# Kernel optimization log

Hardware: AMD Instinct MI355X
Metric: run time of the kernel (lower is better)

Reference implementation:

```python
import jax, jax.numpy as jnp
import numpy as np

NEG_INF = -1e9  # large negative for masking (avoid NaN rows under -inf with fully masked rows)
LEAKY_SLOPE = 0.2

def setup_inputs() -> dict:
    key = jax.random.key(0)
    k1, k2, k3, k4, k5 = jax.random.split(key, 5)
    N, in_dim, out_dim = 8192, 512, 64
    x = jax.random.normal(k1, (N, in_dim), dtype=jnp.float32)
    adj = jax.random.randint(k2, (N, N), 0, 2, dtype=jnp.int32)
    W = jax.random.normal(k3, (out_dim, in_dim), dtype=jnp.float32) * (1.0 / np.sqrt(in_dim))
    a_src = jax.random.normal(k4, (out_dim,), dtype=jnp.float32)
    a_dst = jax.random.normal(k5, (out_dim,), dtype=jnp.float32)
    return {"x": x, "adj": adj, "W": W, "a_src": a_src, "a_dst": a_dst}

def reference(x, adj, W, a_src, a_dst):
    # Linear projection: Wh[n, d]
    Wh = x @ W.T
    # Additive GAT attention: e[i, j] = LeakyReLU(a_src . Wh_i + a_dst . Wh_j)
    s = Wh @ a_src  # [N]
    d = Wh @ a_dst  # [N]
    e = jax.nn.leaky_relu(s[:, None] + d[None, :], negative_slope=LEAKY_SLOPE)  # [N, N]
    e = jnp.where(adj > 0, e, NEG_INF)
    alpha = jax.nn.softmax(e, axis=1)  # [N, N]
    # Dropout on alpha is identity in eval/reference mode.
    h_prime = alpha @ Wh  # [N, out_dim]
    return h_prime
```

## Files before the change

### kernel.cpp

```cpp
#include <hip/hip_runtime.h>
#include <hip/hip_bf16.h>

#define GN 8192
#define IN_DIM 512
#define ODIM 64
#define SLOPE 0.2f
#define JSPLIT 16
#define JCH (GN / JSPLIT)
#define NTILE 4

typedef __attribute__((ext_vector_type(4))) float  f32x4;
typedef __attribute__((ext_vector_type(4))) int    i32x4;
typedef __attribute__((ext_vector_type(8))) short  bf16x8;
typedef __attribute__((ext_vector_type(4))) unsigned short u16x4;

static __device__ __forceinline__ float bf2f(unsigned short u) {
    return __uint_as_float(((unsigned)u) << 16);
}
static __device__ __forceinline__ unsigned short f2bf(float f) {
    union { float f; unsigned u; } c; c.f = f;
    unsigned b = c.u;
    return (unsigned short)((b + 0x7fffu + ((b >> 16) & 1u)) >> 16);
}

static __device__ __forceinline__ bf16x8 load8(const void* p, size_t off, int f32) {
    if (f32) {
        f32x4 lo = *(const f32x4*)((const float*)p + off);
        f32x4 hi = *(const f32x4*)((const float*)p + off + 4);
        bf16x8 r;
        #pragma unroll
        for (int q = 0; q < 4; ++q) {
            r[q]     = (short)f2bf(lo[q]);
            r[4 + q] = (short)f2bf(hi[q]);
        }
        return r;
    }
    return *(const bf16x8*)((const ushort*)p + off);
}

extern "C" __global__ __launch_bounds__(256)
void gat_proj(const void* __restrict__ x_, const void* __restrict__ W_,
              const void* __restrict__ as_, const void* __restrict__ ad_,
              ushort* __restrict__ WhTp, float* __restrict__ s_arr,
              float* __restrict__ E1, float* __restrict__ E2,
              int* __restrict__ dmax_bits, int* __restrict__ dflag,
              float* __restrict__ accum, float* __restrict__ lsum)
{
    {
        f32x4 z = {0.f, 0.f, 0.f, 0.f};
        f32x4* ap = (f32x4*)(accum + (size_t)blockIdx.x * 4096);
        #pragma unroll
        for (int k = 0; k < 4; ++k) ap[k * 256 + threadIdx.x] = z;
        if (threadIdx.x < 64) lsum[blockIdx.x * 64 + threadIdx.x] = 0.f;
    }
    const int wave = threadIdx.x >> 6;
    const int lane = threadIdx.x & 63;
    unsigned xw = ((const unsigned*)x_)[lane];
    unsigned ef = (xw >> 23) & 0xffu;
    unsigned long long vt = __ballot(ef > 60u && ef < 180u);
    const int f32 = (__popcll(vt) >= 32) ? 1 : 0;
    if (blockIdx.x == 0 && threadIdx.x == 0) *dflag = f32;

    const int quad = lane >> 4;
    const int lq   = lane & 15;
    const int i0   = blockIdx.x * 64 + wave * 16;

    f32x4 acc[4] = {{0,0,0,0},{0,0,0,0},{0,0,0,0},{0,0,0,0}};
    const size_t arow = (size_t)(i0 + lq) * IN_DIM;
    #pragma unroll 2
    for (int k0 = 0; k0 < IN_DIM; k0 += 32) {
        const int kk = k0 + quad * 8;
        bf16x8 a  = load8(x_, arow + kk, f32);
        bf16x8 b0 = load8(W_, (size_t)( 0 + lq) * IN_DIM + kk, f32);
        bf16x8 b1 = load8(W_, (size_t)(16 + lq) * IN_DIM + kk, f32);
        bf16x8 b2 = load8(W_, (size_t)(32 + lq) * IN_DIM + kk, f32);
        bf16x8 b3 = load8(W_, (size_t)(48 + lq) * IN_DIM + kk, f32);
        acc[0] = __builtin_amdgcn_mfma_f32_16x16x32_bf16(a, b0, acc[0], 0, 0, 0);
        acc[1] = __builtin_amdgcn_mfma_f32_16x16x32_bf16(a, b1, acc[1], 0, 0, 0);
        acc[2] = __builtin_amdgcn_mfma_f32_16x16x32_bf16(a, b2, acc[2], 0, 0, 0);
        acc[3] = __builtin_amdgcn_mfma_f32_16x16x32_bf16(a, b3, acc[3], 0, 0, 0);
    }
    float av_s[4], av_d[4];
    #pragma unroll
    for (int t = 0; t < 4; ++t) {
        const int n = t * 16 + lq;
        av_s[t] = f32 ? ((const float*)as_)[n] : bf2f(((const ushort*)as_)[n]);
        av_d[t] = f32 ? ((const float*)ad_)[n] : bf2f(((const ushort*)ad_)[n]);
    }
    #pragma unroll
    for (int t = 0; t < 4; ++t) {
        u16x4 pk;
        #pragma unroll
        for (int r = 0; r < 4; ++r) pk[r] = f2bf(acc[t][r]);
        const size_t hw = ((size_t)((i0 >> 3) + (quad >> 1)) * 64 + t * 16 + lq) * 8
                          + (quad & 1) * 4;
        *(u16x4*)(WhTp + hw) = pk;
    }
    float ps[4], pd[4];
    #pragma unroll
    for (int r = 0; r < 4; ++r) {
        float s = 0.f, d = 0.f;
        #pragma unroll
        for (int t = 0; t < 4; ++t) {
            s = fmaf(acc[t][r], av_s[t], s);
            d = fmaf(acc[t][r], av_d[t], d);
        }
        #pragma unroll
        for (int off = 1; off < 16; off <<= 1) {
            s += __shfl_xor(s, off);
            d += __shfl_xor(d, off);
        }
        ps[r] = s; pd[r] = d;
    }
    if (lq == 0) {
        float dmx = -1e30f;
        #pragma unroll
        for (int r = 0; r < 4; ++r) {
            const int n = i0 + quad * 4 + r;
            const float dv = pd[r];
            s_arr[n] = ps[r];
            E1[n] = __expf(fminf(dv, 87.f));
            E2[n] = __expf(SLOPE * dv);
            dmx = fmaxf(dmx, dv);
        }
        if (dmx > 0.f) atomicMax(dmax_bits, __float_as_int(dmx));
    }
}

extern "C" __global__ __launch_bounds__(256)
void gat_attn(const int* __restrict__ adj, const ushort* __restrict__ WhTp,
              const float* __restrict__ s_arr,
              const float* __restrict__ E1, const float* __restrict__ E2,
              const int* __restrict__ dmax_bits,
              float* __restrict__ accum, float* __restrict__ lsum)
{
    const int b    = blockIdx.x;
    const int ib   = 127 - (b & 127);
    const int js0  = b >> 7;
    const int wave = threadIdx.x >> 6;
    const int lane = threadIdx.x & 63;
    const int quad = lane >> 4;
    const int lq   = lane & 15;
    const int i0   = ib * 64;
    const int i    = i0 + wave * 16 + lq;

    const float dmax = __int_as_float(*dmax_bits);
    const float si  = s_arr[i];
    const float tbv = si + dmax;
    const float mi  = fmaxf(tbv, SLOPE * tbv);
    const float Aw  = __expf(si - mi);
    const float Bw  = __expf(SLOPE * si - mi);

    const size_t rowbase = (size_t)i * GN + quad * 8;

    #define COLOF(u) ((js0 + 4 * (NTILE - 1 - ((u) >> 4))) * JCH + ((u) & 15) * 32)

    i32x4 ra[4], rb[4];

    f32x4 acc0 = {0,0,0,0}, acc1 = {0,0,0,0}, acc2 = {0,0,0,0}, acc3 = {0,0,0,0};
    f32x4 acc4 = {0,0,0,0};
    bf16x8 ones;
    #pragma unroll
    for (int q = 0; q < 8; ++q) ones[q] = (short)0x3F80;

    #pragma unroll
    for (int c = 0; c < 4; ++c) {
        const int* p = adj + rowbase + COLOF(c);
        ra[c] = ((const i32x4*)p)[0];
        rb[c] = ((const i32x4*)p)[1];
    }
    f32x4 e1a, e1b, e2a, e2b;
    bf16x8 b0, b1, b2, b3;
    {
        const int col = COLOF(0);
        const float* p1 = E1 + col + quad * 8;
        const float* p2 = E2 + col + quad * 8;
        e1a = *(const f32x4*)p1; e1b = *(const f32x4*)(p1 + 4);
        e2a = *(const f32x4*)p2; e2b = *(const f32x4*)(p2 + 4);
        const ushort* nb = WhTp + ((size_t)(col >> 3) + quad) * 512;
        b0 = *(const bf16x8*)(nb + ( 0 + lq) * 8);
        b1 = *(const bf16x8*)(nb + (16 + lq) * 8);
        b2 = *(const bf16x8*)(nb + (32 + lq) * 8);
        b3 = *(const bf16x8*)(nb + (48 + lq) * 8);
    }

    #pragma unroll 1
    for (int t = 0; t < NTILE; ++t) {
        #pragma unroll
        for (int it = 0; it < 16; ++it) {
            const int u = t * 16 + it;
            const i32x4 va = ra[it & 3], vb = rb[it & 3];
            if (t < NTILE - 1 || it < 12) {
                const int* p = adj + rowbase + COLOF(u + 4);
                ra[it & 3] = ((const i32x4*)p)[0];
                rb[it & 3] = ((const i32x4*)p)[1];
            }
            const int un  = (u < NTILE * 16 - 1) ? u + 1 : u;
            const int ncol = COLOF(un);
            const float* p1 = E1 + ncol + quad * 8;
            const float* p2 = E2 + ncol + quad * 8;
            f32x4 ne1a = *(const f32x4*)p1, ne1b = *(const f32x4*)(p1 + 4);
            f32x4 ne2a = *(const f32x4*)p2, ne2b = *(const f32x4*)(p2 + 4);
            const ushort* nb = WhTp + ((size_t)(ncol >> 3) + quad) * 512;
            bf16x8 nb0 = *(const bf16x8*)(nb + ( 0 + lq) * 8);
            bf16x8 nb1 = *(const bf16x8*)(nb + (16 + lq) * 8);
            bf16x8 nb2 = *(const bf16x8*)(nb + (32 + lq) * 8);
            bf16x8 nb3 = *(const bf16x8*)(nb + (48 + lq) * 8);
            float w[8];
            #pragma unroll
            for (int q = 0; q < 4; ++q) {
                const float w0 = fmaxf(Aw * e1a[q], Bw * e2a[q]);
                const float w1 = fmaxf(Aw * e1b[q], Bw * e2b[q]);
                w[q]     = (va[q] > 0) ? w0 : 0.f;
                w[4 + q] = (vb[q] > 0) ? w1 : 0.f;
            }
            union { bf16x8 v; __hip_bfloat162 h[4]; } af;
            #pragma unroll
            for (int q = 0; q < 4; ++q)
                af.h[q] = __float22bfloat162_rn(make_float2(w[2 * q], w[2 * q + 1]));
            acc0 = __builtin_amdgcn_mfma_f32_16x16x32_bf16(af.v, b0, acc0, 0, 0, 0);
            acc1 = __builtin_amdgcn_mfma_f32_16x16x32_bf16(af.v, b1, acc1, 0, 0, 0);
            acc2 = __builtin_amdgcn_mfma_f32_16x16x32_bf16(af.v, b2, acc2, 0, 0, 0);
            acc3 = __builtin_amdgcn_mfma_f32_16x16x32_bf16(af.v, b3, acc3, 0, 0, 0);
            acc4 = __builtin_amdgcn_mfma_f32_16x16x32_bf16(af.v, ones, acc4, 0, 0, 0);
            e1a = ne1a; e1b = ne1b; e2a = ne2a; e2b = ne2b;
            b0 = nb0; b1 = nb1; b2 = nb2; b3 = nb3;
        }
    }
    #undef COLOF

    const int orow = i0 + wave * 16 + quad * 4;
    if (lq == 0) {
        #pragma unroll
        for (int r = 0; r < 4; ++r) atomicAdd(&lsum[orow + r], acc4[r]);
    }
    #pragma unroll
    for (int r = 0; r < 4; ++r) {
        atomicAdd(&accum[(size_t)(orow + r) * ODIM +  0 + lq], acc0[r]);
        atomicAdd(&accum[(size_t)(orow + r) * ODIM + 16 + lq], acc1[r]);
        atomicAdd(&accum[(size_t)(orow + r) * ODIM + 32 + lq], acc2[r]);
        atomicAdd(&accum[(size_t)(orow + r) * ODIM + 48 + lq], acc3[r]);
    }
}

extern "C" __global__ __launch_bounds__(256)
void gat_final(const float* __restrict__ accum, const float* __restrict__ lsum,
               const int* __restrict__ flag, void* __restrict__ out)
{
    const int idx = blockIdx.x * 256 + threadIdx.x;
    const float v = accum[idx] / lsum[idx >> 6];
    if (*flag) ((float*)out)[idx] = v;
    else       ((ushort*)out)[idx] = f2bf(v);
}

extern "C" void kernel_launch(void* const* d_in, const int* in_sizes, int n_in,
                              void* d_out, int out_size, void* d_ws, size_t ws_size,
                              hipStream_t stream)
{
    const void* x     = d_in[0];
    const int*  adj   = (const int*)d_in[1];
    const void* W     = d_in[2];
    const void* a_src = d_in[3];
    const void* a_dst = d_in[4];

    char* ws = (char*)d_ws;
    size_t off = 0;
    int* dmax_bits = (int*)(ws + off);  off += 128;
    int* dflag = (int*)(ws + off);      off += 128;
    size_t zero_bytes = off;
    float* accum = (float*)(ws + off);  off += (size_t)GN * ODIM * 4;
    float* lsum  = (float*)(ws + off);  off += (size_t)GN * 4;
    float* s_arr = (float*)(ws + off);  off += (size_t)GN * 4;
    float* E1    = (float*)(ws + off);  off += (size_t)GN * 4;
    float* E2    = (float*)(ws + off);  off += (size_t)GN * 4;
    ushort* WhTp = (ushort*)(ws + off); off += (size_t)ODIM * GN * 2;

    hipMemsetAsync(ws, 0, zero_bytes, stream);
    gat_proj<<<GN / 64, 256, 0, stream>>>(x, W, a_src, a_dst,
                                          WhTp, s_arr, E1, E2, dmax_bits, dflag,
                                          accum, lsum);
    gat_attn<<<512, 256, 0, stream>>>(adj, WhTp, s_arr, E1, E2,
                                      dmax_bits, accum, lsum);
    gat_final<<<GN * ODIM / 256, 256, 0, stream>>>(accum, lsum, dflag, d_out);
}
```

Before: 447.3 us.

## Stage E1/E2 in LDS and deepen prefetch of adjacency and Wh tiles

The attention kernel now copies the block's E1/E2 column slice into shared memory once at kernel start, replacing per-iteration global loads. Adjacency prefetch depth grows from 4 to 8 tiles and the Wh B-operand prefetch grows from 1 to 4 tiles ahead, using register ring buffers. The aim is to hide more global-memory latency on the adj stream, which dominates, at the cost of more VGPRs and possibly lower occupancy, plus one barrier.

```diff
diff --git a/kernel.cpp b/kernel.cpp
--- a/kernel.cpp
+++ b/kernel.cpp
@@ -36,6 +36,14 @@
         return r;
     }
     return *(const bf16x8*)((const ushort*)p + off);
+}
+
+static __device__ __forceinline__ int colof(int js0, int u) {
+    return (js0 + 4 * (NTILE - 1 - (u >> 4))) * JCH + (u & 15) * 32;
+}
+static __device__ __forceinline__ int colof2(int js0, int t, int itx) {
+    const int tt = t + (itx >> 4);
+    return (js0 + 4 * (NTILE - 1 - tt)) * JCH + (itx & 15) * 32;
 }
 
 extern "C" __global__ __launch_bounds__(256)
@@ -134,6 +142,7 @@
               const int* __restrict__ dmax_bits,
               float* __restrict__ accum, float* __restrict__ lsum)
 {
+    __shared__ float lE[2 * NTILE * 512];
     const int b    = blockIdx.x;
     const int ib   = 127 - (b & 127);
     const int js0  = b >> 7;
@@ -144,6 +153,15 @@
     const int i0   = ib * 64;
     const int i    = i0 + wave * 16 + lq;
 
+    {
+        const int m0 = threadIdx.x * 8;
+        const int gcol = colof(js0, m0 >> 5) + (m0 & 31);
+        *(f32x4*)&lE[m0]            = *(const f32x4*)(E1 + gcol);
+        *(f32x4*)&lE[m0 + 4]        = *(const f32x4*)(E1 + gcol + 4);
+        *(f32x4*)&lE[2048 + m0]     = *(const f32x4*)(E2 + gcol);
+        *(f32x4*)&lE[2048 + m0 + 4] = *(const f32x4*)(E2 + gcol + 4);
+    }
+
     const float dmax = __int_as_float(*dmax_bits);
     const float si  = s_arr[i];
     const float tbv = si + dmax;
@@ -153,9 +171,8 @@
 
     const size_t rowbase = (size_t)i * GN + quad * 8;
 
-    #define COLOF(u) ((js0 + 4 * (NTILE - 1 - ((u) >> 4))) * JCH + ((u) & 15) * 32)
-
-    i32x4 ra[4], rb[4];
+    i32x4 ra[8], rb[8];
+    bf16x8 w0r[4], w1r[4], w2r[4], w3r[4];
 
     f32x4 acc0 = {0,0,0,0}, acc1 = {0,0,0,0}, acc2 = {0,0,0,0}, acc3 = {0,0,0,0};
     f32x4 acc4 = {0,0,0,0};
@@ -165,47 +182,47 @@
 
     #pragma unroll
     for (int c = 0; c < 4; ++c) {
-        const int* p = adj + rowbase + COLOF(c);
+        const int col = colof(js0, c);
+        const ushort* nb = WhTp + ((size_t)(col >> 3) + quad) * 512;
+        w0r[c] = *(const bf16x8*)(nb + ( 0 + lq) * 8);
+        w1r[c] = *(const bf16x8*)(nb + (16 + lq) * 8);
+        w2r[c] = *(const bf16x8*)(nb + (32 + lq) * 8);
+        w3r[c] = *(const bf16x8*)(nb + (48 + lq) * 8);
+    }
+    #pragma unroll
+    for (int c = 0; c < 8; ++c) {
+        const int* p = adj + rowbase + colof(js0, c);
         ra[c] = ((const i32x4*)p)[0];
         rb[c] = ((const i32x4*)p)[1];
     }
-    f32x4 e1a, e1b, e2a, e2b;
-    bf16x8 b0, b1, b2, b3;
-    {
-        const int col = COLOF(0);
-        const float* p1 = E1 + col + quad * 8;
-        const float* p2 = E2 + col + quad * 8;
-        e1a = *(const f32x4*)p1; e1b = *(const f32x4*)(p1 + 4);
-        e2a = *(const f32x4*)p2; e2b = *(const f32x4*)(p2 + 4);
-        const ushort* nb = WhTp + ((size_t)(col >> 3) + quad) * 512;
-        b0 = *(const bf16x8*)(nb + ( 0 + lq) * 8);
-        b1 = *(const bf16x8*)(nb + (16 + lq) * 8);
-        b2 = *(const bf16x8*)(nb + (32 + lq) * 8);
-        b3 = *(const bf16x8*)(nb + (48 + lq) * 8);
-    }
+    __syncthreads();
 
     #pragma unroll 1
     for (int t = 0; t < NTILE; ++t) {
         #pragma unroll
         for (int it = 0; it < 16; ++it) {
             const int u = t * 16 + it;
-            const i32x4 va = ra[it & 3], vb = rb[it & 3];
-            if (t < NTILE - 1 || it < 12) {
-                const int* p = adj + rowbase + COLOF(u + 4);
-                ra[it & 3] = ((const i32x4*)p)[0];
-                rb[it & 3] = ((const i32x4*)p)[1];
+            bf16x8 cb0 = w0r[it & 3], cb1 = w1r[it & 3];
+            bf16x8 cb2 = w2r[it & 3], cb3 = w3r[it & 3];
+            if ((t < NTILE - 1) || (it < 12)) {
+                const int col = colof2(js0, t, it + 4);
+                const ushort* nb = WhTp + ((size_t)(col >> 3) + quad) * 512;
+                w0r[it & 3] = *(const bf16x8*)(nb + ( 0 + lq) * 8);
+                w1r[it & 3] = *(const bf16x8*)(nb + (16 + lq) * 8);
+                w2r[it & 3] = *(const bf16x8*)(nb + (32 + lq) * 8);
+                w3r[it & 3] = *(const bf16x8*)(nb + (48 + lq) * 8);
             }
-            const int un  = (u < NTILE * 16 - 1) ? u + 1 : u;
-            const int ncol = COLOF(un);
-            const float* p1 = E1 + ncol + quad * 8;
-            const float* p2 = E2 + ncol + quad * 8;
-            f32x4 ne1a = *(const f32x4*)p1, ne1b = *(const f32x4*)(p1 + 4);
-            f32x4 ne2a = *(const f32x4*)p2, ne2b = *(const f32x4*)(p2 + 4);
-            const ushort* nb = WhTp + ((size_t)(ncol >> 3) + quad) * 512;
-            bf16x8 nb0 = *(const bf16x8*)(nb + ( 0 + lq) * 8);
-            bf16x8 nb1 = *(const bf16x8*)(nb + (16 + lq) * 8);
-            bf16x8 nb2 = *(const bf16x8*)(nb + (32 + lq) * 8);
-            bf16x8 nb3 = *(const bf16x8*)(nb + (48 + lq) * 8);
+            const i32x4 va = ra[it & 7], vb = rb[it & 7];
+            if ((t < NTILE - 1) || (it < 8)) {
+                const int* p = adj + rowbase + colof2(js0, t, it + 8);
+                ra[it & 7] = ((const i32x4*)p)[0];
+                rb[it & 7] = ((const i32x4*)p)[1];
+            }
+            const float* pe = lE + u * 32 + quad * 8;
+            const f32x4 e1a = *(const f32x4*)pe;
+            const f32x4 e1b = *(const f32x4*)(pe + 4);
+            const f32x4 e2a = *(const f32x4*)(pe + 2048);
+            const f32x4 e2b = *(const f32x4*)(pe + 2052);
             float w[8];
             #pragma unroll
             for (int q = 0; q < 4; ++q) {
@@ -218,16 +235,13 @@
             #pragma unroll
             for (int q = 0; q < 4; ++q)
                 af.h[q] = __float22bfloat162_rn(make_float2(w[2 * q], w[2 * q + 1]));
-            acc0 = __builtin_amdgcn_mfma_f32_16x16x32_bf16(af.v, b0, acc0, 0, 0, 0);
-            acc1 = __builtin_amdgcn_mfma_f32_16x16x32_bf16(af.v, b1, acc1, 0, 0, 0);
-            acc2 = __builtin_amdgcn_mfma_f32_16x16x32_bf16(af.v, b2, acc2, 0, 0, 0);
-            acc3 = __builtin_amdgcn_mfma_f32_16x16x32_bf16(af.v, b3, acc3, 0, 0, 0);
+            acc0 = __builtin_amdgcn_mfma_f32_16x16x32_bf16(af.v, cb0, acc0, 0, 0, 0);
+            acc1 = __builtin_amdgcn_mfma_f32_16x16x32_bf16(af.v, cb1, acc1, 0, 0, 0);
+            acc2 = __builtin_amdgcn_mfma_f32_16x16x32_bf16(af.v, cb2, acc2, 0, 0, 0);
+            acc3 = __builtin_amdgcn_mfma_f32_16x16x32_bf16(af.v, cb3, acc3, 0, 0, 0);
             acc4 = __builtin_amdgcn_mfma_f32_16x16x32_bf16(af.v, ones, acc4, 0, 0, 0);
-            e1a = ne1a; e1b = ne1b; e2a = ne2a; e2b = ne2b;
-            b0 = nb0; b1 = nb1; b2 = nb2; b3 = nb3;
-        }
-    }
-    #undef COLOF
+        }
+    }
 
     const int orow = i0 + wave * 16 + quad * 4;
     if (lq == 0) {
```

New measurement: 446.4 us. About the same (-0.2%).

## Pack adjacency into a bitmask and stage E1/E2 in LDS for attention

Applied to the files above, without the earlier changes.

Adds a pre-pass kernel that compresses the int32 adjacency matrix into a one-bit-per-edge mask with fully coalesced reads. The attention kernel then reads 4 bytes of mask per 32 columns instead of 128 bytes of int32, and loads the E1/E2 exponent tables once into shared memory. The attention grid doubles to 1024 blocks, each covering contiguous 1024-column spans. The full adjacency matrix is still read once, so the gain depends on the pack kernel streaming better than the old strided per-row loads did.

```diff
diff --git a/kernel.cpp b/kernel.cpp
--- a/kernel.cpp
+++ b/kernel.cpp
@@ -5,9 +5,8 @@
 #define IN_DIM 512
 #define ODIM 64
 #define SLOPE 0.2f
-#define JSPLIT 16
-#define JCH (GN / JSPLIT)
-#define NTILE 4
+#define NT2 2
+#define JSPLIT2 8
 
 typedef __attribute__((ext_vector_type(4))) float  f32x4;
 typedef __attribute__((ext_vector_type(4))) int    i32x4;
@@ -36,6 +35,22 @@
         return r;
     }
     return *(const bf16x8*)((const ushort*)p + off);
+}
+
+extern "C" __global__ __launch_bounds__(256)
+void gat_pack(const int* __restrict__ adj, unsigned* __restrict__ gbm)
+{
+    const size_t ui = (size_t)blockIdx.x * 256 + threadIdx.x;
+    const int* p = adj + ui * 32;
+    unsigned w = 0;
+    #pragma unroll
+    for (int c = 0; c < 8; ++c) {
+        i32x4 v = ((const i32x4*)p)[c];
+        #pragma unroll
+        for (int q = 0; q < 4; ++q)
+            w |= (v[q] > 0 ? 1u : 0u) << (c * 4 + q);
+    }
+    gbm[ui] = w;
 }
 
 extern "C" __global__ __launch_bounds__(256)
@@ -128,14 +143,16 @@
 }
 
 extern "C" __global__ __launch_bounds__(256)
-void gat_attn(const int* __restrict__ adj, const ushort* __restrict__ WhTp,
+void gat_attn(const unsigned char* __restrict__ gbm,
+              const ushort* __restrict__ WhTp,
               const float* __restrict__ s_arr,
               const float* __restrict__ E1, const float* __restrict__ E2,
               const int* __restrict__ dmax_bits,
               float* __restrict__ accum, float* __restrict__ lsum)
 {
+    __shared__ float lE[2 * NT2 * 512];
     const int b    = blockIdx.x;
-    const int ib   = 127 - (b & 127);
+    const int ib   = b & 127;
     const int js0  = b >> 7;
     const int wave = threadIdx.x >> 6;
     const int lane = threadIdx.x & 63;
@@ -144,6 +161,13 @@
     const int i0   = ib * 64;
     const int i    = i0 + wave * 16 + lq;
 
+    {
+        const int m0 = threadIdx.x * 4;
+        const int gcol = (js0 * NT2 + (m0 >> 9)) * 512 + (m0 & 511);
+        *(f32x4*)&lE[m0]        = *(const f32x4*)(E1 + gcol);
+        *(f32x4*)&lE[1024 + m0] = *(const f32x4*)(E2 + gcol);
+    }
+
     const float dmax = __int_as_float(*dmax_bits);
     const float si  = s_arr[i];
     const float tbv = si + dmax;
@@ -151,11 +175,8 @@
     const float Aw  = __expf(si - mi);
     const float Bw  = __expf(SLOPE * si - mi);
 
-    const size_t rowbase = (size_t)i * GN + quad * 8;
-
-    #define COLOF(u) ((js0 + 4 * (NTILE - 1 - ((u) >> 4))) * JCH + ((u) & 15) * 32)
-
-    i32x4 ra[4], rb[4];
+    const unsigned char* mrow = gbm + (size_t)i * (GN / 8);
+    const int colbase = js0 * NT2 * 512;
 
     f32x4 acc0 = {0,0,0,0}, acc1 = {0,0,0,0}, acc2 = {0,0,0,0}, acc3 = {0,0,0,0};
     f32x4 acc4 = {0,0,0,0};
@@ -163,56 +184,44 @@
     #pragma unroll
     for (int q = 0; q < 8; ++q) ones[q] = (short)0x3F80;
 
-    #pragma unroll
-    for (int c = 0; c < 4; ++c) {
-        const int* p = adj + rowbase + COLOF(c);
-        ra[c] = ((const i32x4*)p)[0];
-        rb[c] = ((const i32x4*)p)[1];
-    }
-    f32x4 e1a, e1b, e2a, e2b;
+    unsigned bm = *(const unsigned*)(mrow + (colbase >> 3));
     bf16x8 b0, b1, b2, b3;
     {
-        const int col = COLOF(0);
-        const float* p1 = E1 + col + quad * 8;
-        const float* p2 = E2 + col + quad * 8;
-        e1a = *(const f32x4*)p1; e1b = *(const f32x4*)(p1 + 4);
-        e2a = *(const f32x4*)p2; e2b = *(const f32x4*)(p2 + 4);
+        const int col = colbase;
         const ushort* nb = WhTp + ((size_t)(col >> 3) + quad) * 512;
         b0 = *(const bf16x8*)(nb + ( 0 + lq) * 8);
         b1 = *(const bf16x8*)(nb + (16 + lq) * 8);
         b2 = *(const bf16x8*)(nb + (32 + lq) * 8);
         b3 = *(const bf16x8*)(nb + (48 + lq) * 8);
     }
+    __syncthreads();
 
     #pragma unroll 1
-    for (int t = 0; t < NTILE; ++t) {
+    for (int t = 0; t < NT2; ++t) {
         #pragma unroll
         for (int it = 0; it < 16; ++it) {
             const int u = t * 16 + it;
-            const i32x4 va = ra[it & 3], vb = rb[it & 3];
-            if (t < NTILE - 1 || it < 12) {
-                const int* p = adj + rowbase + COLOF(u + 4);
-                ra[it & 3] = ((const i32x4*)p)[0];
-                rb[it & 3] = ((const i32x4*)p)[1];
-            }
-            const int un  = (u < NTILE * 16 - 1) ? u + 1 : u;
-            const int ncol = COLOF(un);
-            const float* p1 = E1 + ncol + quad * 8;
-            const float* p2 = E2 + ncol + quad * 8;
-            f32x4 ne1a = *(const f32x4*)p1, ne1b = *(const f32x4*)(p1 + 4);
-            f32x4 ne2a = *(const f32x4*)p2, ne2b = *(const f32x4*)(p2 + 4);
+            const int un   = (u < NT2 * 16 - 1) ? u + 1 : u;
+            const int ncol = colbase + un * 32;
+            const unsigned nbm = *(const unsigned*)(mrow + (ncol >> 3));
             const ushort* nb = WhTp + ((size_t)(ncol >> 3) + quad) * 512;
-            bf16x8 nb0 = *(const bf16x8*)(nb + ( 0 + lq) * 8);
-            bf16x8 nb1 = *(const bf16x8*)(nb + (16 + lq) * 8);
-            bf16x8 nb2 = *(const bf16x8*)(nb + (32 + lq) * 8);
-            bf16x8 nb3 = *(const bf16x8*)(nb + (48 + lq) * 8);
+            const bf16x8 nb0 = *(const bf16x8*)(nb + ( 0 + lq) * 8);
+            const bf16x8 nb1 = *(const bf16x8*)(nb + (16 + lq) * 8);
+            const bf16x8 nb2 = *(const bf16x8*)(nb + (32 + lq) * 8);
+            const bf16x8 nb3 = *(const bf16x8*)(nb + (48 + lq) * 8);
+            const float* pe = lE + u * 32 + quad * 8;
+            const f32x4 e1a = *(const f32x4*)pe;
+            const f32x4 e1b = *(const f32x4*)(pe + 4);
+            const f32x4 e2a = *(const f32x4*)(pe + 1024);
+            const f32x4 e2b = *(const f32x4*)(pe + 1028);
+            const unsigned m8 = (bm >> (quad * 8)) & 0xffu;
             float w[8];
             #pragma unroll
             for (int q = 0; q < 4; ++q) {
                 const float w0 = fmaxf(Aw * e1a[q], Bw * e2a[q]);
                 const float w1 = fmaxf(Aw * e1b[q], Bw * e2b[q]);
-                w[q]     = (va[q] > 0) ? w0 : 0.f;
-                w[4 + q] = (vb[q] > 0) ? w1 : 0.f;
+                w[q]     = ((m8 >> q) & 1u) ? w0 : 0.f;
+                w[4 + q] = ((m8 >> (4 + q)) & 1u) ? w1 : 0.f;
             }
             union { bf16x8 v; __hip_bfloat162 h[4]; } af;
             #pragma unroll
@@ -223,11 +232,9 @@
             acc2 = __builtin_amdgcn_mfma_f32_16x16x32_bf16(af.v, b2, acc2, 0, 0, 0);
             acc3 = __builtin_amdgcn_mfma_f32_16x16x32_bf16(af.v, b3, acc3, 0, 0, 0);
             acc4 = __builtin_amdgcn_mfma_f32_16x16x32_bf16(af.v, ones, acc4, 0, 0, 0);
-            e1a = ne1a; e1b = ne1b; e2a = ne2a; e2b = ne2b;
-            b0 = nb0; b1 = nb1; b2 = nb2; b3 = nb3;
-        }
-    }
-    #undef COLOF
+            bm = nbm; b0 = nb0; b1 = nb1; b2 = nb2; b3 = nb3;
+        }
+    }
 
     const int orow = i0 + wave * 16 + quad * 4;
     if (lq == 0) {
@@ -274,12 +281,15 @@
     float* E1    = (float*)(ws + off);  off += (size_t)GN * 4;
     float* E2    = (float*)(ws + off);  off += (size_t)GN * 4;
     ushort* WhTp = (ushort*)(ws + off); off += (size_t)ODIM * GN * 2;
+    unsigned* gbm = (unsigned*)(ws + off); off += (size_t)GN * (GN / 8);
 
     hipMemsetAsync(ws, 0, zero_bytes, stream);
+    gat_pack<<<GN * (GN / 32) / 256, 256, 0, stream>>>(adj, gbm);
     gat_proj<<<GN / 64, 256, 0, stream>>>(x, W, a_src, a_dst,
                                           WhTp, s_arr, E1, E2, dmax_bits, dflag,
                                           accum, lsum);
-    gat_attn<<<512, 256, 0, stream>>>(adj, WhTp, s_arr, E1, E2,
-                                      dmax_bits, accum, lsum);
+    gat_attn<<<128 * JSPLIT2, 256, 0, stream>>>((const unsigned char*)gbm, WhTp,
+                                                s_arr, E1, E2, dmax_bits,
+                                                accum, lsum);
     gat_final<<<GN * ODIM / 256, 256, 0, stream>>>(accum, lsum, dflag, d_out);
 }
```

Measured after the change: 460.9 us. 1.03x slower.
